# Performance work log

Hardware: AMD Instinct MI355X
Metric: run time of the kernel (lower is better)

The kernel has to match this reference:

```python
import jax, jax.numpy as jnp
import numpy as np

D_MODEL = 1024
NUM_HEADS = 16
D_HEAD = D_MODEL // NUM_HEADS


def setup_inputs() -> dict:
    key = jax.random.key(0)
    ks = jax.random.split(key, 9)
    B, L, E = 2, 2048, D_MODEL
    bound = 1.0 / np.sqrt(E)  # torch nn.Linear init range
    inp = {
        "query": jax.random.normal(ks[0], (B, L, E), dtype=jnp.float32),
        "key": jax.random.normal(ks[1], (B, L, E), dtype=jnp.float32),
        "value": jax.random.normal(ks[2], (B, L, E), dtype=jnp.float32),
        "wq": jax.random.uniform(ks[3], (E, E), jnp.float32, -bound, bound),
        "bq": jax.random.uniform(ks[4], (E,), jnp.float32, -bound, bound),
        "wk": jax.random.uniform(ks[5], (E, E), jnp.float32, -bound, bound),
        "bk": jax.random.uniform(ks[6], (E,), jnp.float32, -bound, bound),
        "wv": jax.random.uniform(ks[7], (E, E), jnp.float32, -bound, bound),
        "bv": jax.random.uniform(ks[8], (E,), jnp.float32, -bound, bound),
    }
    return inp


def reference(query, key, value, wq, bq, wk, bk, wv, bv):
    B, L, E = query.shape
    H, Dh = NUM_HEADS, D_HEAD
    scale = Dh ** 0.5
    # linear projections (torch Linear: x @ W.T + b)
    q = (query @ wq.T + bq).reshape(B, L, H, Dh).transpose(0, 2, 1, 3)  # bhld
    k = (key @ wk.T + bk).reshape(B, L, H, Dh).transpose(0, 2, 1, 3)
    v = (value @ wv.T + bv).reshape(B, L, H, Dh).transpose(0, 2, 1, 3)
    scores = jnp.einsum("bhld,bhsd->bhls", q, k) / scale
    attn = jax.nn.softmax(scores, axis=-1)  # dropout p=0 / eval: identity
    out = jnp.einsum("bhls,bhsd->bhld", attn, v)
    return out.transpose(0, 2, 1, 3).reshape(B, L, E)
```

## Files before the change

### kernel.cpp

```cpp
#include <hip/hip_runtime.h>
#include <hip/hip_bf16.h>


typedef __attribute__((ext_vector_type(8))) short short8;
typedef __attribute__((ext_vector_type(4))) short short4v;
typedef __attribute__((ext_vector_type(4))) float floatx4;

#define L_SEQ 2048
#define EMB 1024
#define NH 16
#define DH 64
#define QSCALE 0.18033688011112042f

__device__ __forceinline__ void gl16(const void* g, void* l) {
  __builtin_amdgcn_global_load_lds(
      (const __attribute__((address_space(1))) void*)g,
      (__attribute__((address_space(3))) void*)l, 16, 0, 0);
}

__global__ void cvt6_kernel(const float* __restrict__ s0, const float* __restrict__ s1,
                            const float* __restrict__ s2, const float* __restrict__ s3,
                            const float* __restrict__ s4, const float* __restrict__ s5,
                            __hip_bfloat16* __restrict__ d0, __hip_bfloat16* __restrict__ d1,
                            __hip_bfloat16* __restrict__ d2, __hip_bfloat16* __restrict__ d3,
                            __hip_bfloat16* __restrict__ d4, __hip_bfloat16* __restrict__ d5,
                            int nx8, int nw8) {
  const int t = blockIdx.y;
  const float* src = (t == 0) ? s0 : (t == 1) ? s1 : (t == 2) ? s2
                   : (t == 3) ? s3 : (t == 4) ? s4 : s5;
  __hip_bfloat16* dst = (t == 0) ? d0 : (t == 1) ? d1 : (t == 2) ? d2
                      : (t == 3) ? d3 : (t == 4) ? d4 : d5;
  const int n8 = (t < 3) ? nx8 : nw8;
  int i = blockIdx.x * blockDim.x + threadIdx.x;
  const int stride = gridDim.x * blockDim.x;
  for (; i < n8; i += stride) {
    const float4* s4p = (const float4*)src;
    float4 a = s4p[2 * i];
    float4 b = s4p[2 * i + 1];
    union { short8 v; __hip_bfloat16 h[8]; } u;
    u.h[0] = __float2bfloat16(a.x); u.h[1] = __float2bfloat16(a.y);
    u.h[2] = __float2bfloat16(a.z); u.h[3] = __float2bfloat16(a.w);
    u.h[4] = __float2bfloat16(b.x); u.h[5] = __float2bfloat16(b.y);
    u.h[6] = __float2bfloat16(b.z); u.h[7] = __float2bfloat16(b.w);
    *(short8*)(dst + 8 * i) = u.v;
  }
}

#define CPAD 136
__global__ __launch_bounds__(256) void proj_kernel(
    const __hip_bfloat16* __restrict__ xq, const __hip_bfloat16* __restrict__ xk,
    const __hip_bfloat16* __restrict__ xv,
    const __hip_bfloat16* __restrict__ wqb, const __hip_bfloat16* __restrict__ wkb,
    const __hip_bfloat16* __restrict__ wvb,
    const float* __restrict__ bq, const float* __restrict__ bk,
    const float* __restrict__ bv,
    __hip_bfloat16* __restrict__ Qb, __hip_bfloat16* __restrict__ Kb,
    __hip_bfloat16* __restrict__ Vt) {
  __shared__ __align__(16) __hip_bfloat16 lds[128 * CPAD];
  const int tid = threadIdx.x;
  const int bx = blockIdx.x;
  const int by = blockIdx.y;
  const int p = by >> 3;
  const int n0 = (by & 7) * 128;
  const int m0 = bx * 128;
  const __hip_bfloat16* X = (p == 0) ? xq : (p == 1) ? xk : xv;
  const __hip_bfloat16* W = (p == 0) ? wqb : (p == 1) ? wkb : wvb;
  const float* bias = (p == 0) ? bq : (p == 1) ? bk : bv;

  const int w = tid >> 6, ln = tid & 63;
  const int wm = w & 1, wn = w >> 1;
  const int quad = ln >> 4, lr = ln & 15;

  floatx4 acc[4][4];
#pragma unroll
  for (int i = 0; i < 4; ++i)
#pragma unroll
    for (int j = 0; j < 4; ++j) acc[i][j] = (floatx4){0.f, 0.f, 0.f, 0.f};

  const int srow = tid >> 3;
  const int scol = (((tid & 7) ^ ((tid >> 3) & 7)) * 8);

  for (int kt = 0; kt < 16; ++kt) {
    const int k0 = kt * 64;
#pragma unroll
    for (int i = 0; i < 4; ++i) {
      gl16(X + (size_t)(m0 + i * 32 + srow) * EMB + k0 + scol,
           lds + i * 2048 + tid * 8);
      gl16(W + (size_t)(n0 + i * 32 + srow) * EMB + k0 + scol,
           lds + 8192 + i * 2048 + tid * 8);
    }
    __syncthreads();
#pragma unroll
    for (int ks = 0; ks < 2; ++ks) {
      short8 af[4], bf[4];
#pragma unroll
      for (int mt = 0; mt < 4; ++mt)
        af[mt] = *(const short8*)(lds + (wm * 64 + mt * 16 + lr) * 64 +
                                  (((ks * 4 + quad) ^ (lr & 7)) * 8));
#pragma unroll
      for (int nt = 0; nt < 4; ++nt)
        bf[nt] = *(const short8*)(lds + 8192 + (wn * 64 + nt * 16 + lr) * 64 +
                                  (((ks * 4 + quad) ^ (lr & 7)) * 8));
#pragma unroll
      for (int mt = 0; mt < 4; ++mt)
#pragma unroll
        for (int nt = 0; nt < 4; ++nt)
          acc[mt][nt] = __builtin_amdgcn_mfma_f32_16x16x32_bf16(
              af[mt], bf[nt], acc[mt][nt], 0, 0, 0);
    }
    __syncthreads();
  }

  if (p == 2) {
#pragma unroll
    for (int nt = 0; nt < 4; ++nt) {
      const int nl = wn * 64 + nt * 16 + lr;
      const float bb = bias[n0 + nl];
#pragma unroll
      for (int mt = 0; mt < 4; ++mt) {
        union { short4v v; __hip_bfloat16 h4[4]; } u;
#pragma unroll
        for (int r = 0; r < 4; ++r) u.h4[r] = __float2bfloat16(acc[mt][nt][r] + bb);
        *(short4v*)(&lds[nl * CPAD + wm * 64 + mt * 16 + quad * 4]) = u.v;
      }
    }
  } else {
    const float scl = (p == 0) ? QSCALE : 1.0f;
#pragma unroll
    for (int nt = 0; nt < 4; ++nt) {
      const int nl = wn * 64 + nt * 16 + lr;
      const float bb = bias[n0 + nl];
#pragma unroll
      for (int mt = 0; mt < 4; ++mt)
#pragma unroll
        for (int r = 0; r < 4; ++r)
          lds[(wm * 64 + mt * 16 + quad * 4 + r) * CPAD + nl] =
              __float2bfloat16((acc[mt][nt][r] + bb) * scl);
    }
  }
  __syncthreads();

  {
    const int tr = tid >> 1, half = tid & 1;
    const int b = m0 >> 11;
    const __hip_bfloat16* src = lds + tr * CPAD + half * 64;
    __hip_bfloat16* g;
    if (p == 2) {
      const int ng = n0 + tr;
      const int h = ng >> 6, d = ng & 63;
      g = Vt + ((size_t)((b * NH + h) * DH + d)) * L_SEQ + (m0 & 2047) + half * 64;
    } else {
      __hip_bfloat16* dst = (p == 0) ? Qb : Kb;
      const int m = m0 + tr;
      const int h = (n0 >> 6) + half;
      g = dst + ((size_t)((b * NH + h) * L_SEQ + (m & 2047))) * DH;
    }
#pragma unroll
    for (int j = 0; j < 8; ++j)
      *(short8*)(g + j * 8) = *(const short8*)(src + j * 8);
  }
}

__global__ __launch_bounds__(256, 2) void attn_kernel(
    const __hip_bfloat16* __restrict__ Qb, const __hip_bfloat16* __restrict__ Kb,
    const __hip_bfloat16* __restrict__ Vt, float* __restrict__ out) {
  __shared__ __align__(16) __hip_bfloat16 Kl[2][4096];
  __shared__ __align__(16) __hip_bfloat16 Vl[2][4096];
  __shared__ __align__(16) __hip_bfloat16 Pl[4][2048];

  const int tid = threadIdx.x;
  const int w = tid >> 6, ln = tid & 63;
  const int quad = ln >> 4, lr = ln & 15;
  const int bh = blockIdx.y;
  const int q0 = blockIdx.x * 128 + w * 32;
  const __hip_bfloat16* Qp = Qb + (size_t)bh * L_SEQ * DH;
  const __hip_bfloat16* Kp = Kb + (size_t)bh * L_SEQ * DH;
  const __hip_bfloat16* Vp = Vt + (size_t)bh * DH * L_SEQ;

  short8 qf[2][2];
#pragma unroll
  for (int qs = 0; qs < 2; ++qs)
#pragma unroll
    for (int kk = 0; kk < 2; ++kk)
      qf[qs][kk] = *(const short8*)(Qp + (size_t)(q0 + qs * 16 + lr) * DH + kk * 32 + quad * 8);

  int koff[2], voff[2], loff[2];
#pragma unroll
  for (int i = 0; i < 2; ++i) {
    const int idx = i * 256 + tid;
    const int srow = idx >> 3;
    const int c = (idx & 7) ^ (srow & 7);
    koff[i] = srow * DH + c * 8;
    voff[i] = srow * L_SEQ + c * 8;
    loff[i] = idx * 8;
  }

  floatx4 acc[2][4];
  float psum[2];
#pragma unroll
  for (int qs = 0; qs < 2; ++qs) {
    psum[qs] = 0.f;
#pragma unroll
    for (int nt = 0; nt < 4; ++nt) acc[qs][nt] = (floatx4){0.f, 0.f, 0.f, 0.f};
  }

#pragma unroll
  for (int i = 0; i < 2; ++i) gl16(Kp + koff[i], &Kl[0][loff[i]]);
#pragma unroll
  for (int i = 0; i < 2; ++i) gl16(Vp + voff[i], &Vl[0][loff[i]]);

  const int xsw = lr & 7;
  const int xswp = (lr & 7) ^ ((lr >> 3) << 2);

  for (int it = 0; it < 32; ++it) {
    __syncthreads();
    if (it + 1 < 32) {
      const int s0 = (it + 1) * 64;
      const int bf = (it + 1) & 1;
#pragma unroll
      for (int i = 0; i < 2; ++i) gl16(Kp + (size_t)s0 * DH + koff[i], &Kl[bf][loff[i]]);
#pragma unroll
      for (int i = 0; i < 2; ++i) gl16(Vp + s0 + voff[i], &Vl[bf][loff[i]]);
    }
    const __hip_bfloat16* Kt = Kl[it & 1];
    const __hip_bfloat16* Vtile = Vl[it & 1];

#pragma unroll
    for (int mt = 0; mt < 4; ++mt) {
      floatx4 sc[2];
#pragma unroll
      for (int qs = 0; qs < 2; ++qs) sc[qs] = (floatx4){0.f, 0.f, 0.f, 0.f};
#pragma unroll
      for (int kk = 0; kk < 2; ++kk) {
        const short8 kf = *(const short8*)(Kt + ((mt * 16 + lr) * 8 + ((kk * 4 + quad) ^ xsw)) * 8);
#pragma unroll
        for (int qs = 0; qs < 2; ++qs)
          sc[qs] = __builtin_amdgcn_mfma_f32_16x16x32_bf16(kf, qf[qs][kk], sc[qs], 0, 0, 0);
      }
      const int cch = mt * 2 + (quad >> 1);
#pragma unroll
      for (int qs = 0; qs < 2; ++qs) {
        union { short4v v; __hip_bfloat16 h4[4]; } u;
#pragma unroll
        for (int r = 0; r < 4; ++r) {
          const float pv = __builtin_amdgcn_exp2f(sc[qs][r]);
          psum[qs] += pv;
          u.h4[r] = __float2bfloat16(pv);
        }
        const int row = qs * 16 + lr;
        *(short4v*)(&Pl[w][row * 64 + ((cch ^ xswp) * 8 + (quad & 1) * 4)]) = u.v;
      }
    }

#pragma unroll
    for (int kk = 0; kk < 2; ++kk) {
      short8 vf[4];
#pragma unroll
      for (int nt = 0; nt < 4; ++nt)
        vf[nt] = *(const short8*)(Vtile + ((nt * 16 + lr) * 8 + ((kk * 4 + quad) ^ xsw)) * 8);
#pragma unroll
      for (int qs = 0; qs < 2; ++qs) {
        const short8 pf = *(const short8*)(&Pl[w][(qs * 16 + lr) * 64 + ((kk * 4 + quad) ^ xswp) * 8]);
#pragma unroll
        for (int nt = 0; nt < 4; ++nt)
          acc[qs][nt] = __builtin_amdgcn_mfma_f32_16x16x32_bf16(pf, vf[nt], acc[qs][nt], 0, 0, 0);
      }
    }
  }

#pragma unroll
  for (int qs = 0; qs < 2; ++qs) {
    psum[qs] += __shfl_xor(psum[qs], 16, 64);
    psum[qs] += __shfl_xor(psum[qs], 32, 64);
  }

  const int b = bh >> 4, h = bh & 15;
#pragma unroll
  for (int qs = 0; qs < 2; ++qs) {
#pragma unroll
    for (int r = 0; r < 4; ++r) {
      const float inv = 1.0f / __shfl(psum[qs], quad * 4 + r, 64);
      const int lq = q0 + qs * 16 + quad * 4 + r;
#pragma unroll
      for (int nt = 0; nt < 4; ++nt)
        out[((size_t)(b * L_SEQ + lq)) * EMB + h * DH + nt * 16 + lr] = acc[qs][nt][r] * inv;
    }
  }
}

extern "C" void kernel_launch(void* const* d_in, const int* in_sizes, int n_in,
                              void* d_out, int out_size, void* d_ws, size_t ws_size,
                              hipStream_t stream) {
  const float* xq = (const float*)d_in[0];
  const float* xk = (const float*)d_in[1];
  const float* xv = (const float*)d_in[2];
  const float* wq = (const float*)d_in[3];
  const float* bq = (const float*)d_in[4];
  const float* wk = (const float*)d_in[5];
  const float* bk = (const float*)d_in[6];
  const float* wv = (const float*)d_in[7];
  const float* bv = (const float*)d_in[8];

  const size_t NX = (size_t)4096 * 1024;
  const size_t NW = (size_t)1024 * 1024;
  __hip_bfloat16* xbq = (__hip_bfloat16*)d_ws;
  __hip_bfloat16* xbk = xbq + NX;
  __hip_bfloat16* xbv = xbk + NX;
  __hip_bfloat16* wbq = xbv + NX;
  __hip_bfloat16* wbk = wbq + NW;
  __hip_bfloat16* wbv = wbk + NW;
  __hip_bfloat16* Qb = wbv + NW;
  __hip_bfloat16* Kb = Qb + NX;
  __hip_bfloat16* Vt = Kb + NX;

  cvt6_kernel<<<dim3(1024, 6), 256, 0, stream>>>(xq, xk, xv, wq, wk, wv,
                                                 xbq, xbk, xbv, wbq, wbk, wbv,
                                                 (int)(NX / 8), (int)(NW / 8));

  proj_kernel<<<dim3(32, 24), 256, 0, stream>>>(xbq, xbk, xbv, wbq, wbk, wbv,
                                                bq, bk, bv, Qb, Kb, Vt);
  attn_kernel<<<dim3(16, 32), 256, 0, stream>>>(Qb, Kb, Vt, (float*)d_out);
}
```

Measured before the change: 199.5 us.

## Split attention over key halves with atomic accumulation and separate normalization

```diff
diff --git a/kernel.cpp b/kernel.cpp
--- a/kernel.cpp
+++ b/kernel.cpp
@@ -161,9 +161,10 @@
   }
 }
 
-__global__ __launch_bounds__(256, 2) void attn_kernel(
+__global__ __launch_bounds__(256, 4) void attn_kernel(
     const __hip_bfloat16* __restrict__ Qb, const __hip_bfloat16* __restrict__ Kb,
-    const __hip_bfloat16* __restrict__ Vt, float* __restrict__ out) {
+    const __hip_bfloat16* __restrict__ Vt, float* __restrict__ out,
+    float* __restrict__ psP) {
   __shared__ __align__(16) __hip_bfloat16 Kl[2][4096];
   __shared__ __align__(16) __hip_bfloat16 Vl[2][4096];
   __shared__ __align__(16) __hip_bfloat16 Pl[4][2048];
@@ -172,6 +173,8 @@
   const int w = tid >> 6, ln = tid & 63;
   const int quad = ln >> 4, lr = ln & 15;
   const int bh = blockIdx.y;
+  const int sh = blockIdx.z;
+  const int sbase = sh * 1024;
   const int q0 = blockIdx.x * 128 + w * 32;
   const __hip_bfloat16* Qp = Qb + (size_t)bh * L_SEQ * DH;
   const __hip_bfloat16* Kp = Kb + (size_t)bh * L_SEQ * DH;
@@ -205,17 +208,17 @@
   }
 
 #pragma unroll
-  for (int i = 0; i < 2; ++i) gl16(Kp + koff[i], &Kl[0][loff[i]]);
-#pragma unroll
-  for (int i = 0; i < 2; ++i) gl16(Vp + voff[i], &Vl[0][loff[i]]);
+  for (int i = 0; i < 2; ++i) gl16(Kp + (size_t)sbase * DH + koff[i], &Kl[0][loff[i]]);
+#pragma unroll
+  for (int i = 0; i < 2; ++i) gl16(Vp + sbase + voff[i], &Vl[0][loff[i]]);
 
   const int xsw = lr & 7;
   const int xswp = (lr & 7) ^ ((lr >> 3) << 2);
 
-  for (int it = 0; it < 32; ++it) {
+  for (int it = 0; it < 16; ++it) {
     __syncthreads();
-    if (it + 1 < 32) {
-      const int s0 = (it + 1) * 64;
+    if (it + 1 < 16) {
+      const int s0 = sbase + (it + 1) * 64;
       const int bf = (it + 1) & 1;
 #pragma unroll
       for (int i = 0; i < 2; ++i) gl16(Kp + (size_t)s0 * DH + koff[i], &Kl[bf][loff[i]]);
@@ -274,18 +277,39 @@
     psum[qs] += __shfl_xor(psum[qs], 32, 64);
   }
 
+  if (quad == 0) {
+#pragma unroll
+    for (int qs = 0; qs < 2; ++qs)
+      psP[sh * (32 * L_SEQ) + bh * L_SEQ + q0 + qs * 16 + lr] = psum[qs];
+  }
+
   const int b = bh >> 4, h = bh & 15;
 #pragma unroll
   for (int qs = 0; qs < 2; ++qs) {
 #pragma unroll
     for (int r = 0; r < 4; ++r) {
-      const float inv = 1.0f / __shfl(psum[qs], quad * 4 + r, 64);
       const int lq = q0 + qs * 16 + quad * 4 + r;
 #pragma unroll
       for (int nt = 0; nt < 4; ++nt)
-        out[((size_t)(b * L_SEQ + lq)) * EMB + h * DH + nt * 16 + lr] = acc[qs][nt][r] * inv;
-    }
-  }
+        atomicAdd(&out[((size_t)(b * L_SEQ + lq)) * EMB + h * DH + nt * 16 + lr],
+                  acc[qs][nt][r]);
+    }
+  }
+}
+
+__global__ __launch_bounds__(256) void norm_kernel(float* __restrict__ out,
+                                                   const float* __restrict__ psP) {
+  const int idx4 = blockIdx.x * blockDim.x + threadIdx.x;
+  const int flat = idx4 * 4;
+  const int e = flat & 1023;
+  const int l = (flat >> 10) & 2047;
+  const int b = flat >> 21;
+  const int bh = b * NH + (e >> 6);
+  const float ps = psP[bh * L_SEQ + l] + psP[32 * L_SEQ + bh * L_SEQ + l];
+  const float inv = 1.0f / ps;
+  float4 v = ((float4*)out)[idx4];
+  v.x *= inv; v.y *= inv; v.z *= inv; v.w *= inv;
+  ((float4*)out)[idx4] = v;
 }
 
 extern "C" void kernel_launch(void* const* d_in, const int* in_sizes, int n_in,
@@ -312,6 +336,9 @@
   __hip_bfloat16* Qb = wbv + NW;
   __hip_bfloat16* Kb = Qb + NX;
   __hip_bfloat16* Vt = Kb + NX;
+  float* psP = (float*)xbv;
+
+  hipMemsetAsync(d_out, 0, (size_t)out_size * sizeof(float), stream);
 
   cvt6_kernel<<<dim3(1024, 6), 256, 0, stream>>>(xq, xk, xv, wq, wk, wv,
                                                  xbq, xbk, xbv, wbq, wbk, wbv,
@@ -319,5 +346,6 @@
 
   proj_kernel<<<dim3(32, 24), 256, 0, stream>>>(xbq, xbk, xbv, wbq, wbk, wbv,
                                                 bq, bk, bv, Qb, Kb, Vt);
-  attn_kernel<<<dim3(16, 32), 256, 0, stream>>>(Qb, Kb, Vt, (float*)d_out);
-}
+  attn_kernel<<<dim3(16, 32, 2), 256, 0, stream>>>(Qb, Kb, Vt, (float*)d_out, psP);
+  norm_kernel<<<4096, 256, 0, stream>>>((float*)d_out, psP);
+}
```

New measurement: 221.3 us. 10.9% more time.
